# Kernel optimization log

Measured on AMD Instinct MI355X. Metric: run time of the kernel, lower is better.

## Reference

```python
import jax, jax.numpy as jnp
import numpy as np

K = 7            # neighbor volumes (NNN heads)
PS = 10          # patch size
ADJ = PS // 2    # patch anchor offset (use_adj)
WOFF = 29 // 2   # search window half-size (ws=29)
KSEARCH = 224    # hardcoded in forward
T, C, E, HH, WW = 1, 8, 8, 64, 64


def _box1(a, axis):
    # sliding-window sum of length PS anchored at i-ADJ, zero outside
    pw = [(0, 0)] * a.ndim
    pw[axis] = (ADJ, PS - 1 - ADJ)
    ap = jnp.pad(a, pw)
    c = jnp.cumsum(ap, axis=axis)
    zp = [(0, 0)] * a.ndim
    zp[axis] = (1, 0)
    c = jnp.pad(c, zp)
    n = a.shape[axis]
    return jax.lax.slice_in_dim(c, PS, PS + n, axis=axis) - jax.lax.slice_in_dim(c, 0, n, axis=axis)


def box_sum(a):
    return _box1(_box1(a, -2), -1)


def setup_inputs():
    key = jax.random.key(0)
    ks = jax.random.split(key, 5)
    x = jax.random.normal(ks[0], (T, C, HH, WW), jnp.float32)
    xe = jax.random.normal(ks[1], (T, E, HH, WW), jnp.float32)
    ye = jax.random.normal(ks[2], (T, E, HH, WW), jnp.float32)
    y = jax.random.normal(ks[3], (T, C, HH, WW), jnp.float32)
    log_temp = 0.1 * jax.random.normal(ks[4], (T, 1, HH, WW), jnp.float32)
    return {"x": x, "xe": xe, "ye": ye, "y": y, "log_temp": log_temp}


def reference(x, xe, ye, y, log_temp):
    pad = lambda a: jnp.pad(a, ((0, 0), (0, 0), (1, 1), (1, 1)))
    x, xe, ye, y, log_temp = pad(x), pad(xe), pad(ye), pad(y), pad(log_temp)
    H, W = x.shape[-2:]
    Q = H * W
    xe0, ye0 = xe[0], ye[0]
    # search window offsets (ws x ws)
    dy, dx = np.meshgrid(np.arange(-WOFF, WOFF + 1), np.arange(-WOFF, WOFF + 1), indexing='ij')
    dy = jnp.asarray(dy.ravel()); dx = jnp.asarray(dx.ravel())
    nW = dy.shape[0]  # 841
    # patch squared norms (zero padded patches)
    n2_q = box_sum((ye0 ** 2).sum(0))   # (H,W)
    n2_db = box_sum((xe0 ** 2).sum(0))  # (H,W)
    xep = jnp.pad(xe0, ((0, 0), (WOFF, WOFF), (WOFF, WOFF)))
    n2p = jnp.pad(n2_db, WOFF)
    def shifted(d):
        s = jax.lax.dynamic_slice(xep, (0, WOFF + d[0], WOFF + d[1]), (E, H, W))
        n = jax.lax.dynamic_slice(n2p, (WOFF + d[0], WOFF + d[1]), (H, W))
        return s, n
    xe_s, n2_s = jax.vmap(shifted)(jnp.stack([dy, dx], -1))  # (nW,E,H,W),(nW,H,W)
    cross = box_sum((ye0[None] * xe_s).sum(1))               # (nW,H,W)
    dist = n2_q[None] + n2_s - 2.0 * cross                   # L2^2, (nW,H,W)
    qy = jnp.arange(H)[:, None]; qx = jnp.arange(W)[None, :]
    valid = ((qy[None] + dy[:, None, None] >= 0) & (qy[None] + dy[:, None, None] < H)
             & (qx[None] + dx[:, None, None] >= 0) & (qx[None] + dx[:, None, None] < W))
    self_m = (dy == 0) & (dx == 0)  # remove_self
    dist = jnp.where(valid & ~self_m[:, None, None], dist, 1e10)
    dist = dist.transpose(1, 2, 0).reshape(Q, nW)
    negd, idx = jax.lax.top_k(-dist, KSEARCH)  # closest KSEARCH, negd = -L2
    # avg-pooled log temperature per query patch
    lt = (box_sum(log_temp[0, 0]) / (PS * PS)).reshape(Q)
    # NeuralNearestNeighbors: iterative continuous top-k relaxation
    logits = negd / jnp.exp(lt)[:, None]
    Ws = []
    for _ in range(K):
        w = jax.nn.softmax(logits, axis=-1)
        logits = logits + jnp.log(jnp.clip(1.0 - w, 1e-6, None))
        Ws.append(w)
    Wk = jnp.stack(Ws)  # (K,Q,KSEARCH)
    # absolute candidate coords
    qyf = jnp.repeat(jnp.arange(H), W); qxf = jnp.tile(jnp.arange(W), H)
    ny = qyf[:, None] + dy[idx]; nx = qxf[:, None] + dx[idx]  # (Q,KSEARCH)
    # weighted patch sum (gather per patch offset)
    xpad = jnp.pad(x[0], ((0, 0), (ADJ, PS - 1 - ADJ), (ADJ, PS - 1 - ADJ)))
    z = jnp.zeros((K, Q, C, PS, PS), x.dtype)
    for oy in range(PS):
        for ox in range(PS):
            vals = xpad[:, ny + oy, nx + ox]  # (C,Q,KSEARCH)
            z = z.at[:, :, :, oy, ox].set(jnp.einsum('kqj,cqj->kqc', Wk, vals))
    # fold with counting (iFoldz): overlap-add of patches + coverage counts
    zp = z.transpose(1, 0, 2, 3, 4).reshape(H, W, K * C, PS, PS)
    buf = jnp.zeros((K * C, H + PS - 1, W + PS - 1), x.dtype)
    cnt = jnp.zeros((H + PS - 1, W + PS - 1), x.dtype)
    for oy in range(PS):
        for ox in range(PS):
            buf = buf.at[:, oy:oy + H, ox:ox + W].add(zp[:, :, :, oy, ox].transpose(2, 0, 1))
            cnt = cnt.at[oy:oy + H, ox:ox + W].add(1.0)
    vid = buf[:, ADJ:ADJ + H, ADJ:ADJ + W]
    zvid = cnt[ADJ:ADJ + H, ADJ:ADJ + W]
    zagg = vid / zvid[None]
    zagg = zagg.reshape(T, K, C, H, W) - y.reshape(T, 1, C, H, W)
    zagg = zagg.reshape(T, K * C, H, W)
    out = jnp.concatenate([y, zagg], axis=1)[..., 1:-1, 1:-1]
    return out
```

## Files before the change

### kernel.cpp

```cpp
#include <hip/hip_runtime.h>
#include <hip/hip_bf16.h>

#define HP    66
#define QTOT  (HP*HP)
#define NWIN  29
#define NW    (NWIN*NWIN)
#define KK    7
#define WOFF2 14
#define NZ    15
#define QB    8
#define QBN   545
#define NIT   27
#define NSEG3 198
#define PSTR  4368


__global__ __launch_bounds__(256) void k_prep1(const float* __restrict__ x,
    const float* __restrict__ xe, const float* __restrict__ ye,
    const float* __restrict__ lt, float* __restrict__ ws) {
  int p = blockIdx.x * 256 + threadIdx.x;
  if (p >= QTOT) return;
  int i = p / HP, j = p % HP;
  bool in = (i >= 1 && i < HP-1 && j >= 1 && j < HP-1);
  int src = (i-1)*64 + (j-1);
  float vy[8], vx[8], vv[8];
  float sy = 0.f, sx = 0.f;
#pragma unroll
  for (int e = 0; e < 8; ++e) {
    vy[e] = in ? ye[e*4096 + src] : 0.f;
    vx[e] = in ? xe[e*4096 + src] : 0.f;
    vv[e] = in ? x [e*4096 + src] : 0.f;
    sy += vy[e]*vy[e]; sx += vx[e]*vx[e];
  }
  float4* yp = (float4*)(ws + (size_t)p*8);
  float4* xp = (float4*)(ws + 8*QTOT + (size_t)p*8);
  float4* vp = (float4*)(ws + 16*QTOT + (size_t)p*8);
  yp[0] = make_float4(vy[0], vy[1], vy[2], vy[3]);
  yp[1] = make_float4(vy[4], vy[5], vy[6], vy[7]);
  xp[0] = make_float4(vx[0], vx[1], vx[2], vx[3]);
  xp[1] = make_float4(vx[4], vx[5], vx[6], vx[7]);
  vp[0] = make_float4(vv[0], vv[1], vv[2], vv[3]);
  vp[1] = make_float4(vv[4], vv[5], vv[6], vv[7]);
  ws[24*QTOT + p] = sy;
  ws[25*QTOT + p] = sx;
  ws[26*QTOT + p] = in ? lt[src] : 0.f;
}

__global__ __launch_bounds__(256) void k_prep2(float* __restrict__ ws) {
  int p = blockIdx.x * 256 + threadIdx.x;
  if (p >= QTOT) return;
  int i = p / HP, j = p % HP;
  const float* sqye = ws + 24*QTOT;
  const float* sqxe = ws + 25*QTOT;
  const float* lt66 = ws + 26*QTOT;
  float a = 0.f, b = 0.f, c = 0.f;
  for (int u = -5; u <= 4; ++u) {
    int ii = i + u; if (ii < 0 || ii >= HP) continue;
    for (int v = -5; v <= 4; ++v) {
      int jj = j + v; if (jj < 0 || jj >= HP) continue;
      int o = ii*HP + jj;
      a += sqye[o]; b += sqxe[o]; c += lt66[o];
    }
  }
  ws[27*QTOT + p] = a;
  ws[28*QTOT + p] = b;
  ws[29*QTOT + p] = c * 0.01f;
}

__global__ __launch_bounds__(256) void k_dist(const float* __restrict__ ws,
                                              float* __restrict__ dist) {
  __shared__ float4 s4[QTOT/4];
  __shared__ float h[QTOT];
  float* s = (float*)s4;
  int w = blockIdx.x, tid = threadIdx.x;
  int dy = w / NWIN - WOFF2, dx = w % NWIN - WOFF2;
  const float* yex = ws;
  const float* xex = ws + 8*QTOT;
  const float* n2q  = ws + 27*QTOT;
  const float* n2db = ws + 28*QTOT;
  for (int p = tid; p < QTOT; p += 256) {
    int i = p / HP, j = p % HP;
    int ii = i + dy, jj = j + dx;
    float sv = 0.f;
    if (ii >= 0 && ii < HP && jj >= 0 && jj < HP) {
      int p2 = ii*HP + jj;
      const float4* yp = (const float4*)(yex + (size_t)p*8);
      const float4* xp = (const float4*)(xex + (size_t)p2*8);
      float4 a0 = yp[0], a1 = yp[1], b0 = xp[0], b1 = xp[1];
      sv += a0.x*b0.x; sv += a0.y*b0.y; sv += a0.z*b0.z; sv += a0.w*b0.w;
      sv += a1.x*b1.x; sv += a1.y*b1.y; sv += a1.z*b1.z; sv += a1.w*b1.w;
    }
    s[p] = sv;
  }
  __syncthreads();
  if (tid < NSEG3) {
    int row = tid % HP, seg = tid / HP, c0 = seg*22;
    const float* ar = s + row*HP;
    float* hr = h + row*HP;
    float w9[9]; float sum = 0.f;
#pragma unroll
    for (int t = 0; t < 9; ++t) {
      int jj = c0 - 5 + t;
      float v = (jj >= 0) ? ar[jj] : 0.f;
      w9[t] = v; sum += v;
    }
#pragma unroll
    for (int t = 0; t < 22; ++t) {
      int j = c0 + t, jn = j + 4;
      float nv = (jn < HP) ? ar[jn] : 0.f;
      sum += nv;
      hr[j] = sum;
      sum -= w9[t % 9];
      w9[t % 9] = nv;
    }
  }
  __syncthreads();
  if (tid < NSEG3) {
    int col = tid % HP, seg = tid / HP, r0 = seg*22;
    float w9[9]; float sum = 0.f;
#pragma unroll
    for (int t = 0; t < 9; ++t) {
      int ii = r0 - 5 + t;
      float v = (ii >= 0) ? h[ii*HP + col] : 0.f;
      w9[t] = v; sum += v;
    }
#pragma unroll
    for (int t = 0; t < 22; ++t) {
      int i = r0 + t, in2 = i + 4;
      float nv = (in2 < HP) ? h[in2*HP + col] : 0.f;
      sum += nv;
      float cr = sum;
      int p = i*HP + col;
      int ii = i + dy, jj = col + dx;
      bool valid = (ii >= 0 && ii < HP && jj >= 0 && jj < HP);
      float dv = 1e10f;
      if (valid && !(dy == 0 && dx == 0))
        dv = n2q[p] + n2db[ii*HP + jj] - 2.f * cr;
      s[p] = dv;
      sum -= w9[t % 9];
      w9[t % 9] = nv;
    }
  }
  __syncthreads();
  float4* dq = (float4*)(dist + (size_t)w*QTOT);
  for (int p4 = tid; p4 < QTOT/4; p4 += 256)
    dq[p4] = s4[p4];
}

__global__ __launch_bounds__(256) void k_weights(const float* __restrict__ ws,
    const float* __restrict__ dist, __hip_bfloat16* __restrict__ wf) {
  __shared__ float mh[32], sh[32];
  int tid = threadIdx.x;
  int bid = blockIdx.x;
  int xcd = bid & 7, idx = bid >> 3;
  int qb = (xcd == 0) ? idx : (69 + (xcd-1)*68 + idx);
  int qq = tid & (QB-1);
  int q = qb * QB + qq;
  bool qok = q < QTOT;
  int qs = qok ? q : (QTOT - 1);
  int wg = tid >> 3;
  int wave = tid >> 6;
  float invT = __expf(-ws[29*QTOT + qs]);
  float lv[NIT];
#pragma unroll
  for (int it = 0; it < NIT; ++it) {
    int w = wg + it*32;
    lv[it] = (qok && w < NW) ? (-dist[w*QTOT + qs] * invT) : -3.0e38f;
  }
  for (int k = 0; k < KK; ++k) {
    float pm = -3.0e38f;
#pragma unroll
    for (int it = 0; it < NIT; ++it) pm = fmaxf(pm, lv[it]);
    pm = fmaxf(pm, __shfl_xor(pm, 8, 64));
    pm = fmaxf(pm, __shfl_xor(pm, 16, 64));
    pm = fmaxf(pm, __shfl_xor(pm, 32, 64));
    if ((tid & 63) < QB) mh[wave*QB + qq] = pm;
    __syncthreads();
    float m = fmaxf(fmaxf(mh[qq], mh[QB+qq]), fmaxf(mh[2*QB+qq], mh[3*QB+qq]));
    float psum = 0.f;
#pragma unroll
    for (int it = 0; it < NIT; ++it) psum += __expf(lv[it] - m);
    psum += __shfl_xor(psum, 8, 64);
    psum += __shfl_xor(psum, 16, 64);
    psum += __shfl_xor(psum, 32, 64);
    if ((tid & 63) < QB) sh[wave*QB + qq] = psum;
    __syncthreads();
    float invden = 1.0f / (sh[qq] + sh[QB+qq] + sh[2*QB+qq] + sh[3*QB+qq]);
    size_t kbase = (size_t)k*NW*PSTR + q;
#pragma unroll
    for (int it = 0; it < NIT; ++it) {
      int w = wg + it*32;
      if (qok && w < NW) {
        float wgt = __expf(lv[it] - m) * invden;
        wf[kbase + (size_t)w*PSTR] = __float2bfloat16(wgt);
        if (k < KK-1 && wgt > 1e-9f)
          lv[it] += __logf(fmaxf(1.f - wgt, 1e-6f));
      }
    }
    __syncthreads();
  }
}

__global__ __launch_bounds__(256) void k_boxw(__hip_bfloat16* __restrict__ wfp) {
  __shared__ uint4 au4[546];
  __shared__ uint4 hu4[546];
  int bid = blockIdx.x;
  uint4* plane = (uint4*)(wfp + (size_t)bid*PSTR);
  int tid = threadIdx.x;
  for (int qb = tid; qb < 546; qb += 256)
    au4[qb] = plane[qb];
  __syncthreads();
  const unsigned short* a16 = (const unsigned short*)au4;
  unsigned short* h16 = (unsigned short*)hu4;
  for (int task = tid; task < 396; task += 256) {
    int row = task % HP, seg = task / HP, c0 = seg*11;
    const unsigned short* ar = a16 + row*HP;
    unsigned short* hr = h16 + row*HP;
    float w9[9]; float sum = 0.f;
#pragma unroll
    for (int t = 0; t < 9; ++t) {
      int jj = c0 - 4 + t;
      float v = (jj >= 0) ? __uint_as_float((unsigned)ar[jj] << 16) : 0.f;
      w9[t] = v; sum += v;
    }
#pragma unroll
    for (int t = 0; t < 11; ++t) {
      int j = c0 + t, jn = j + 5;
      float nv = (jn < HP) ? __uint_as_float((unsigned)ar[jn] << 16) : 0.f;
      sum += nv;
      hr[j] = __bfloat16_as_ushort(__float2bfloat16(sum));
      sum -= w9[t % 9];
      w9[t % 9] = nv;
    }
  }
  __syncthreads();
  unsigned short* a16w = (unsigned short*)au4;
  for (int task = tid; task < 396; task += 256) {
    int col = task % HP, seg = task / HP, r0 = seg*11;
    float w9[9]; float sum = 0.f;
#pragma unroll
    for (int t = 0; t < 9; ++t) {
      int ii = r0 - 4 + t;
      float v = (ii >= 0) ? __uint_as_float((unsigned)h16[ii*HP + col] << 16) : 0.f;
      w9[t] = v; sum += v;
    }
#pragma unroll
    for (int t = 0; t < 11; ++t) {
      int i = r0 + t, in2 = i + 5;
      float nv = (in2 < HP) ? __uint_as_float((unsigned)h16[in2*HP + col] << 16) : 0.f;
      sum += nv;
      a16w[i*HP + col] = __bfloat16_as_ushort(__float2bfloat16(sum));
      sum -= w9[t % 9];
      w9[t % 9] = nv;
    }
  }
  __syncthreads();
  for (int qb = tid; qb < 546; qb += 256)
    plane[qb] = au4[qb];
}

__global__ __launch_bounds__(256) void k_contract(const float* __restrict__ ws,
    const unsigned short* __restrict__ wfb, float* __restrict__ accb2) {
  __shared__ float xt[17][44][8];
  int t = blockIdx.x, z = blockIdx.y, k = blockIdx.z, tid = threadIdx.x;
  int I0 = (t >> 2) * 16, J0 = (t & 3) * 16;
  int dylo = -WOFF2 + 2*z;
  int gy0 = I0 + 1 + dylo, gx0 = J0 - 13;
  const float* x66i = ws + 16*QTOT;
  for (int idx = tid; idx < 17*44; idx += 256) {
    int r = idx / 44, cc = idx % 44;
    int gy = gy0 + r, gx = gx0 + cc;
    float4 v0 = make_float4(0.f,0.f,0.f,0.f), v1 = v0;
    if (gy >= 0 && gy < HP && gx >= 0 && gx < HP) {
      const float4* xp = (const float4*)(x66i + (size_t)(gy*HP + gx)*8);
      v0 = xp[0]; v1 = xp[1];
    }
    float4* d = (float4*)&xt[r][cc][0];
    d[0] = v0; d[1] = v1;
  }
  __syncthreads();
  int il = tid >> 4, jl = tid & 15;
  int I = I0 + 1 + il, J = J0 + 1 + jl;
  int pix = I*HP + J;
  float acc[8];
#pragma unroll
  for (int c = 0; c < 8; ++c) acc[c] = 0.f;
  int ndd = (z == NZ-1) ? 1 : 2;
  for (int dd = 0; dd < ndd; ++dd) {
    int wrow = (dylo + dd + WOFF2) * NWIN;
    const unsigned short* wp = wfb + ((size_t)k*NW + wrow)*PSTR + pix;
    unsigned short wv[NWIN];
#pragma unroll
    for (int dxw = 0; dxw < NWIN; ++dxw) wv[dxw] = wp[(size_t)dxw*PSTR];
    int r = il + dd;
#pragma unroll
    for (int dxw = 0; dxw < NWIN; ++dxw) {
      float wgt = __uint_as_float((unsigned)wv[dxw] << 16);
      const float4* xr = (const float4*)&xt[r][jl + dxw][0];
      float4 x0 = xr[0], x1 = xr[1];
      acc[0] += wgt * x0.x; acc[1] += wgt * x0.y;
      acc[2] += wgt * x0.z; acc[3] += wgt * x0.w;
      acc[4] += wgt * x1.x; acc[5] += wgt * x1.y;
      acc[6] += wgt * x1.z; acc[7] += wgt * x1.w;
    }
  }
  int px64 = (I-1)*64 + (J-1);
#pragma unroll
  for (int c = 0; c < 8; ++c)
    accb2[((z*56 + k*8 + c)*4096) + px64] = acc[c];
}

__global__ __launch_bounds__(256) void k_final(const float* __restrict__ y,
    const float* __restrict__ accb2, float* __restrict__ out) {
  int idx = blockIdx.x * 256 + threadIdx.x;
  int ch = idx >> 12, px = idx & 4095;
  if (ch < 8) { out[idx] = y[ch*4096 + px]; return; }
  int kc = ch - 8, c = kc & 7;
  int i = px >> 6, j = px & 63;
  int I = i + 1, J = j + 1;
  int cy = min(I+5, HP-1) - max(I-4, 0) + 1;
  int cx = min(J+5, HP-1) - max(J-4, 0) + 1;
  float s = 0.f;
  for (int z = 0; z < NZ; ++z) s += accb2[(z*56 + kc)*4096 + px];
  out[idx] = s / (float)(cy*cx) - y[c*4096 + px];
}

extern "C" void kernel_launch(void* const* d_in, const int* in_sizes, int n_in,
                              void* d_out, int out_size, void* d_ws, size_t ws_size,
                              hipStream_t stream) {
  const float* x  = (const float*)d_in[0];
  const float* xe = (const float*)d_in[1];
  const float* ye = (const float*)d_in[2];
  const float* y  = (const float*)d_in[3];
  const float* lt = (const float*)d_in[4];
  float* ws   = (float*)d_ws;
  float* dist = ws + 30*QTOT;
  __hip_bfloat16* wf = (__hip_bfloat16*)(dist + (size_t)NW*QTOT);
  float* accb2 = dist;
  float* out = (float*)d_out;

  k_prep1<<<(QTOT + 255)/256, 256, 0, stream>>>(x, xe, ye, lt, ws);
  k_prep2<<<(QTOT + 255)/256, 256, 0, stream>>>(ws);
  k_dist<<<NW, 256, 0, stream>>>(ws, dist);
  k_weights<<<QBN, 256, 0, stream>>>(ws, dist, wf);
  k_boxw<<<KK*NW, 256, 0, stream>>>(wf);
  k_contract<<<dim3(16, NZ, KK), 256, 0, stream>>>(ws, (const unsigned short*)wf, accb2);
  k_final<<<out_size/256, 256, 0, stream>>>(y, accb2, out);
}
```

Before: 144.4 us.

## Store values as bf16 and give each contract block eight window rows

The value tensor x is now packed as bf16 (16 bytes per pixel), and the contraction tile is staged in shared memory as uint4. Each k_contract block now covers 8 dy rows of the search window instead of 2, so the grid's z-dimension drops from 15 to 4. This cuts redundant halo loads, global traffic and partial-sum writes, and shortens the reduction in k_final. In exchange there are far fewer blocks (448 instead of 1680), which lowers parallelism, and the bf16 values lose precision.

```diff
diff --git a/kernel.cpp b/kernel.cpp
--- a/kernel.cpp
+++ b/kernel.cpp
@@ -7,7 +7,7 @@
 #define NW    (NWIN*NWIN)
 #define KK    7
 #define WOFF2 14
-#define NZ    15
+#define NZC   4
 #define QB    8
 #define QBN   545
 #define NIT   27
@@ -34,13 +34,20 @@
   }
   float4* yp = (float4*)(ws + (size_t)p*8);
   float4* xp = (float4*)(ws + 8*QTOT + (size_t)p*8);
-  float4* vp = (float4*)(ws + 16*QTOT + (size_t)p*8);
   yp[0] = make_float4(vy[0], vy[1], vy[2], vy[3]);
   yp[1] = make_float4(vy[4], vy[5], vy[6], vy[7]);
   xp[0] = make_float4(vx[0], vx[1], vx[2], vx[3]);
   xp[1] = make_float4(vx[4], vx[5], vx[6], vx[7]);
-  vp[0] = make_float4(vv[0], vv[1], vv[2], vv[3]);
-  vp[1] = make_float4(vv[4], vv[5], vv[6], vv[7]);
+  unsigned wd[4];
+#pragma unroll
+  for (int e2 = 0; e2 < 4; ++e2) {
+    unsigned lo = __bfloat16_as_ushort(__float2bfloat16(vv[2*e2]));
+    unsigned hi = __bfloat16_as_ushort(__float2bfloat16(vv[2*e2+1]));
+    wd[e2] = lo | (hi << 16);
+  }
+  uint4* xb = (uint4*)(ws + 16*QTOT);
+  uint4 v4; v4.x = wd[0]; v4.y = wd[1]; v4.z = wd[2]; v4.w = wd[3];
+  xb[p] = v4;
   ws[24*QTOT + p] = sy;
   ws[25*QTOT + p] = sx;
   ws[26*QTOT + p] = in ? lt[src] : 0.f;
@@ -261,22 +268,20 @@
 
 __global__ __launch_bounds__(256) void k_contract(const float* __restrict__ ws,
     const unsigned short* __restrict__ wfb, float* __restrict__ accb2) {
-  __shared__ float xt[17][44][8];
+  __shared__ uint4 xt4[23][45];
   int t = blockIdx.x, z = blockIdx.y, k = blockIdx.z, tid = threadIdx.x;
   int I0 = (t >> 2) * 16, J0 = (t & 3) * 16;
-  int dylo = -WOFF2 + 2*z;
+  int dylo = -WOFF2 + 8*z;
+  int ndd = (z == NZC-1) ? 5 : 8;
+  int NRr = 16 + ndd - 1;
   int gy0 = I0 + 1 + dylo, gx0 = J0 - 13;
-  const float* x66i = ws + 16*QTOT;
-  for (int idx = tid; idx < 17*44; idx += 256) {
+  const uint4* xb = (const uint4*)(ws + 16*QTOT);
+  for (int idx = tid; idx < NRr*44; idx += 256) {
     int r = idx / 44, cc = idx % 44;
     int gy = gy0 + r, gx = gx0 + cc;
-    float4 v0 = make_float4(0.f,0.f,0.f,0.f), v1 = v0;
-    if (gy >= 0 && gy < HP && gx >= 0 && gx < HP) {
-      const float4* xp = (const float4*)(x66i + (size_t)(gy*HP + gx)*8);
-      v0 = xp[0]; v1 = xp[1];
-    }
-    float4* d = (float4*)&xt[r][cc][0];
-    d[0] = v0; d[1] = v1;
+    uint4 v = make_uint4(0u, 0u, 0u, 0u);
+    if (gy >= 0 && gy < HP && gx >= 0 && gx < HP) v = xb[gy*HP + gx];
+    xt4[r][cc] = v;
   }
   __syncthreads();
   int il = tid >> 4, jl = tid & 15;
@@ -285,7 +290,6 @@
   float acc[8];
 #pragma unroll
   for (int c = 0; c < 8; ++c) acc[c] = 0.f;
-  int ndd = (z == NZ-1) ? 1 : 2;
   for (int dd = 0; dd < ndd; ++dd) {
     int wrow = (dylo + dd + WOFF2) * NWIN;
     const unsigned short* wp = wfb + ((size_t)k*NW + wrow)*PSTR + pix;
@@ -296,12 +300,15 @@
 #pragma unroll
     for (int dxw = 0; dxw < NWIN; ++dxw) {
       float wgt = __uint_as_float((unsigned)wv[dxw] << 16);
-      const float4* xr = (const float4*)&xt[r][jl + dxw][0];
-      float4 x0 = xr[0], x1 = xr[1];
-      acc[0] += wgt * x0.x; acc[1] += wgt * x0.y;
-      acc[2] += wgt * x0.z; acc[3] += wgt * x0.w;
-      acc[4] += wgt * x1.x; acc[5] += wgt * x1.y;
-      acc[6] += wgt * x1.z; acc[7] += wgt * x1.w;
+      uint4 xv = xt4[r][jl + dxw];
+      acc[0] += wgt * __uint_as_float(xv.x << 16);
+      acc[1] += wgt * __uint_as_float(xv.x & 0xffff0000u);
+      acc[2] += wgt * __uint_as_float(xv.y << 16);
+      acc[3] += wgt * __uint_as_float(xv.y & 0xffff0000u);
+      acc[4] += wgt * __uint_as_float(xv.z << 16);
+      acc[5] += wgt * __uint_as_float(xv.z & 0xffff0000u);
+      acc[6] += wgt * __uint_as_float(xv.w << 16);
+      acc[7] += wgt * __uint_as_float(xv.w & 0xffff0000u);
     }
   }
   int px64 = (I-1)*64 + (J-1);
@@ -321,7 +328,8 @@
   int cy = min(I+5, HP-1) - max(I-4, 0) + 1;
   int cx = min(J+5, HP-1) - max(J-4, 0) + 1;
   float s = 0.f;
-  for (int z = 0; z < NZ; ++z) s += accb2[(z*56 + kc)*4096 + px];
+#pragma unroll
+  for (int z = 0; z < NZC; ++z) s += accb2[(z*56 + kc)*4096 + px];
   out[idx] = s / (float)(cy*cx) - y[c*4096 + px];
 }
 
@@ -344,6 +352,6 @@
   k_dist<<<NW, 256, 0, stream>>>(ws, dist);
   k_weights<<<QBN, 256, 0, stream>>>(ws, dist, wf);
   k_boxw<<<KK*NW, 256, 0, stream>>>(wf);
-  k_contract<<<dim3(16, NZ, KK), 256, 0, stream>>>(ws, (const unsigned short*)wf, accb2);
+  k_contract<<<dim3(16, NZC, KK), 256, 0, stream>>>(ws, (const unsigned short*)wf, accb2);
   k_final<<<out_size/256, 256, 0, stream>>>(y, accb2, out);
 }
```

After: 162.0 us. 1.12x slower.
